# Optimization experiments

Hardware: AMD Instinct MI355X
Metric: run time of the kernel (lower is better)

The kernel has to match this reference:

```python
import jax, jax.numpy as jnp
import numpy as np

IN_DIM = 128
MEM = 128
BRANCH = 8
DEPTH = 6
N = (BRANCH ** (DEPTH + 1) - 1) // (BRANCH - 1)  # 299593 nodes, BFS order


def setup_inputs() -> dict:
    key = jax.random.key(0)
    ks = jax.random.split(key, 9)
    s_in = 1.0 / np.sqrt(IN_DIM)
    s_m = 1.0 / np.sqrt(MEM)
    f32 = jnp.float32
    return {
        "x": jax.random.normal(ks[0], (N, IN_DIM), f32),
        "W_ioux": jax.random.normal(ks[1], (3 * MEM, IN_DIM), f32) * s_in,
        "b_ioux": jax.random.normal(ks[2], (3 * MEM,), f32) * s_in,
        "W_iouh": jax.random.normal(ks[3], (3 * MEM, MEM), f32) * s_m,
        "b_iouh": jax.random.normal(ks[4], (3 * MEM,), f32) * s_m,
        "W_fx": jax.random.normal(ks[5], (MEM, IN_DIM), f32) * s_in,
        "b_fx": jax.random.normal(ks[6], (MEM,), f32) * s_in,
        "W_fh": jax.random.normal(ks[7], (MEM, MEM), f32) * s_m,
        "b_fh": jax.random.normal(ks[8], (MEM,), f32) * s_m,
        "branch": BRANCH,
        "depth": DEPTH,
    }


def reference(x, W_ioux, b_ioux, W_iouh, b_iouh, W_fx, b_fx, W_fh, b_fh, branch, depth):
    """Child-Sum TreeLSTM over a complete `branch`-ary tree of `depth` levels.

    Nodes are stored in BFS order: level l occupies [off(l), off(l+1)) and the
    children of local parent p at level l are contiguous at level l+1, so the
    recursion becomes a bottom-up sweep with one batched step per level.
    Matches torch node_forward exactly (leaf nodes see a single zero child row,
    i.e. h_sum = 0 -> iouh contributes only its bias, and fc_sum = 0).
    """
    mem = W_fh.shape[0]
    off = lambda l: (branch ** l - 1) // (branch - 1)
    c_prev = h_prev = None  # states of level l+1, [branch**(l+1), mem]
    for l in range(depth, -1, -1):
        n_l = branch ** l
        x_l = x[off(l): off(l) + n_l]  # [n_l, in_dim]
        if l == depth:  # leaves
            h_sum = jnp.zeros((n_l, mem), x.dtype)
            fc_sum = jnp.zeros((n_l, mem), x.dtype)
        else:
            c_ch = c_prev.reshape(n_l, branch, mem)
            h_ch = h_prev.reshape(n_l, branch, mem)
            h_sum = h_ch.sum(axis=1)  # child-sum of h
            # per-child forget gate: sigmoid(fh(h_child) + fx(x_parent))
            f = jax.nn.sigmoid(
                jnp.einsum('nbm,km->nbk', h_ch, W_fh) + b_fh
                + (x_l @ W_fx.T + b_fx)[:, None, :]
            )
            fc_sum = (f * c_ch).sum(axis=1)
        iou = x_l @ W_ioux.T + b_ioux + h_sum @ W_iouh.T + b_iouh
        i, o, u = jnp.split(iou, 3, axis=1)
        c_prev = jax.nn.sigmoid(i) * jnp.tanh(u) + fc_sum
        h_prev = jax.nn.sigmoid(o) * jnp.tanh(c_prev)
    return (c_prev, h_prev)  # root state, each [1, mem]
```

## Files before the change

### kernel.cpp

```cpp
#include <hip/hip_runtime.h>
#include <hip/hip_bf16.h>

#define TB 256
#define LOG2E  1.44269504088896f
#define LOG2E2 2.88539008177793f

typedef __attribute__((ext_vector_type(8))) short bf16x8;
typedef __attribute__((ext_vector_type(4))) float f32x4;

__device__ __forceinline__ short bfb(float f){
  unsigned u = __float_as_uint(f);
  u = u + 0x7fffu + ((u >> 16) & 1u);
  return (short)(u >> 16);
}
__device__ __forceinline__ bf16x8 cvt8(float4 a, float4 b){
  bf16x8 r;
  r[0]=bfb(a.x); r[1]=bfb(a.y); r[2]=bfb(a.z); r[3]=bfb(a.w);
  r[4]=bfb(b.x); r[5]=bfb(b.y); r[6]=bfb(b.z); r[7]=bfb(b.w);
  return r;
}
__device__ __forceinline__ float sig2(float arg){
  return __builtin_amdgcn_rcpf(1.f + __builtin_amdgcn_exp2f(arg));
}
__device__ __forceinline__ float tanh2(float arg){
  return 1.f - 2.f*__builtin_amdgcn_rcpf(1.f + __builtin_amdgcn_exp2f(arg));
}

#define GLD16(gp, lp) __builtin_amdgcn_global_load_lds( \
    (const __attribute__((address_space(1))) void*)(gp), \
    (__attribute__((address_space(3))) void*)(lp), 16, 0, 0)

__global__ __launch_bounds__(TB)
void k_prep(const float* __restrict__ Wioux, const float* __restrict__ Wiouh,
            const float* __restrict__ Wfx,   const float* __restrict__ Wfh,
            const float* __restrict__ bioux, const float* __restrict__ biouh,
            short* __restrict__ WxG, short* __restrict__ WhG,
            short* __restrict__ WfxP, short* __restrict__ WfhP,
            float* __restrict__ biasS){
  const int q = blockIdx.x*TB + threadIdx.x;
  const int t = q >> 8, rem = q & 255;
  const int kf = rem >> 6, lane = rem & 63;
  const int row = t*16 + (lane & 15);
  const int col = kf*32 + (lane >> 4)*8;
  const size_t src = (size_t)row*128 + col;
  if (q < 6144){
    const int g = t & 7, kind = t >> 3;
    const size_t dst = ((size_t)(g*3 + kind)*4 + kf)*512 + (size_t)lane*8;
    const float4* p  = (const float4*)(Wioux + src);
    *(bf16x8*)(WxG + dst) = cvt8(p[0], p[1]);
    const float4* p2 = (const float4*)(Wiouh + src);
    *(bf16x8*)(WhG + dst) = cvt8(p2[0], p2[1]);
  }
  if (q < 2048){
    const size_t dst = ((size_t)t*4 + kf)*512 + (size_t)lane*8;
    const float4* p  = (const float4*)(Wfx + src);
    *(bf16x8*)(WfxP + dst) = cvt8(p[0], p[1]);
    const float4* p2 = (const float4*)(Wfh + src);
    *(bf16x8*)(WfhP + dst) = cvt8(p2[0], p2[1]);
  }
  if (q < 384){
    const float s = (q < 256) ? -LOG2E : LOG2E2;
    biasS[q] = s*(bioux[q] + biouh[q]);
  }
}

__global__ __launch_bounds__(TB, 4)
void k_fx(const float* __restrict__ x, const short* __restrict__ WfxP,
          const float* __restrict__ bfx, const float* __restrict__ bfh,
          float* __restrict__ FXS, int nrows){
  const int tid = threadIdx.x, wave = tid >> 6, lane = tid & 63;
  const int l15 = lane & 15, lhi = lane >> 4;
  const int mrow = (blockIdx.x*4 + wave)*16;
  const int arow = min(mrow + l15, nrows - 1);
  bf16x8 ax[4];
  const float* rp = x + (size_t)arow*128;
  #pragma unroll
  for (int kf = 0; kf < 4; ++kf){
    const float4* p = (const float4*)(rp + kf*32 + lhi*8);
    ax[kf] = cvt8(p[0], p[1]);
  }
  #pragma unroll
  for (int t = 0; t < 8; ++t){
    f32x4 acc = {0.f,0.f,0.f,0.f};
    #pragma unroll
    for (int kf = 0; kf < 4; ++kf){
      bf16x8 b = *(const bf16x8*)(WfxP + ((size_t)(t*4 + kf)*64 + lane)*8);
      acc = __builtin_amdgcn_mfma_f32_16x16x32_bf16(ax[kf], b, acc, 0,0,0);
    }
    const int col = t*16 + l15;
    const float bc = bfx[col] + bfh[col];
    #pragma unroll
    for (int r = 0; r < 4; ++r){
      const int row = mrow + lhi*4 + r;
      if (row < nrows) FXS[(size_t)row*128 + col] = -LOG2E*(acc[r] + bc);
    }
  }
}

__global__ __launch_bounds__(TB, 4)
void k_leaf(const float* __restrict__ x, int xoff,
            const short* __restrict__ WxG, const short* __restrict__ WfhP,
            const float* __restrict__ biasS, const float* __restrict__ FXS,
            int poff, short* __restrict__ HSout, float* __restrict__ FCout)
{
  __shared__ __align__(16) short wbuf[2][6144];
  __shared__ __align__(16) short hbuf[4][2048];
  const int tid = threadIdx.x;
  const int wave = tid >> 6, lane = tid & 63;
  const int l15 = lane & 15, lhi = lane >> 4;
  const int mrow = (blockIdx.x*4 + wave)*16;

  bf16x8 ax[4];
  {
    const float* rp = x + (size_t)(xoff + mrow + l15)*128;
    #pragma unroll
    for (int kf = 0; kf < 4; ++kf){
      const float4* p = (const float4*)(rp + kf*32 + lhi*8);
      ax[kf] = cvt8(p[0], p[1]);
    }
  }

  #define STAGE_L(g, b) { \
    _Pragma("unroll") \
    for (int c = 0; c < 3; ++c){ \
      const int ch = c*4 + wave; \
      GLD16(WxG + (size_t)(g)*6144 + ch*512 + lane*8, &wbuf[b][ch*512]); \
    } }

  STAGE_L(0, 0);

  float cv[8][4];
  const int colb = l15*2;
  const int p = (mrow >> 3) + (lhi >> 1);
  const float* fxp = FXS + (size_t)(poff + p)*128 + l15;

  #pragma unroll
  for (int tt = 0; tt < 8; ++tt){
    __syncthreads();
    if (tt < 7) STAGE_L(tt+1, (tt+1)&1);
    const short* wb = wbuf[tt & 1];

    f32x4 ai = {0.f,0.f,0.f,0.f}, ao = ai, au = ai;
    #pragma unroll
    for (int kf = 0; kf < 4; ++kf){
      bf16x8 bi = *(const bf16x8*)(wb + 0*2048 + kf*512 + lane*8);
      bf16x8 bo = *(const bf16x8*)(wb + 1*2048 + kf*512 + lane*8);
      bf16x8 bu = *(const bf16x8*)(wb + 2*2048 + kf*512 + lane*8);
      ai = __builtin_amdgcn_mfma_f32_16x16x32_bf16(ax[kf], bi, ai, 0,0,0);
      ao = __builtin_amdgcn_mfma_f32_16x16x32_bf16(ax[kf], bo, ao, 0,0,0);
      au = __builtin_amdgcn_mfma_f32_16x16x32_bf16(ax[kf], bu, au, 0,0,0);
    }

    const int col = tt*16 + l15;
    const float bis = biasS[col], bos = biasS[128 + col], bus = biasS[256 + col];
    const int colx = colb + tt*32;
    float hs = 0.f;
    #pragma unroll
    for (int r = 0; r < 4; ++r){
      const int row = lhi*4 + r;
      const float iv = sig2 (__builtin_fmaf(ai[r], -LOG2E, bis));
      const float uv = tanh2(__builtin_fmaf(au[r],  LOG2E2, bus));
      const float ov = sig2 (__builtin_fmaf(ao[r], -LOG2E, bos));
      const float c  = iv*uv;
      const float h  = ov*tanh2(LOG2E2*c);
      cv[tt][r] = c;
      hs += h;
      const int byte = row*256 + (colx ^ (row << 4));
      *(short*)((char*)hbuf[wave] + byte) = bfb(h);
    }
    hs += __shfl_xor(hs, 16);
    if ((lhi & 1) == 0)
      HSout[(size_t)p*128 + col] = bfb(hs);
  }

  bf16x8 af[4];
  #pragma unroll
  for (int kf = 0; kf < 4; ++kf){
    const int byte = l15*256 + (((kf*32 + lhi*8)*2) ^ (l15 << 4));
    af[kf] = *(const bf16x8*)((const char*)hbuf[wave] + byte);
  }
  #pragma unroll
  for (int t2 = 0; t2 < 8; ++t2){
    f32x4 fa = {0.f,0.f,0.f,0.f};
    #pragma unroll
    for (int kf = 0; kf < 4; ++kf){
      bf16x8 b = *(const bf16x8*)(WfhP + ((size_t)(t2*4 + kf)*64 + lane)*8);
      fa = __builtin_amdgcn_mfma_f32_16x16x32_bf16(af[kf], b, fa, 0,0,0);
    }
    const float fxv = fxp[t2*16];
    float fs = 0.f;
    #pragma unroll
    for (int r = 0; r < 4; ++r){
      const float f = sig2(__builtin_fmaf(fa[r], -LOG2E, fxv));
      fs += f * cv[t2][r];
    }
    fs += __shfl_xor(fs, 16);
    if ((lhi & 1) == 0)
      FCout[(size_t)p*128 + t2*16 + l15] = fs;
  }
  #undef STAGE_L
}

__global__ __launch_bounds__(TB, 2)
void k_node(const float* __restrict__ x, int xoff,
            const short* __restrict__ HSin, const float* __restrict__ FCin,
            const short* __restrict__ WxG, const short* __restrict__ WhG,
            const short* __restrict__ WfhP,
            const float* __restrict__ biasS, const float* __restrict__ FXS,
            int poff, short* __restrict__ HSout, float* __restrict__ FCout,
            float* __restrict__ dout, int nnodes)
{
  __shared__ __align__(16) short wbuf[2][12288];
  __shared__ __align__(16) short hbuf[4][2048];
  const int tid = threadIdx.x;
  const int wave = tid >> 6, lane = tid & 63;
  const int l15 = lane & 15, lhi = lane >> 4;
  const int mrow = (blockIdx.x*4 + wave)*16;
  const int arow = min(mrow + l15, nnodes - 1);

  bf16x8 ax[4], ah[4];
  {
    const float* rp = x + (size_t)(xoff + arow)*128;
    #pragma unroll
    for (int kf = 0; kf < 4; ++kf){
      const float4* p = (const float4*)(rp + kf*32 + lhi*8);
      ax[kf] = cvt8(p[0], p[1]);
    }
    const short* hp = HSin + (size_t)arow*128;
    #pragma unroll
    for (int kf = 0; kf < 4; ++kf)
      ah[kf] = *(const bf16x8*)(hp + kf*32 + lhi*8);
  }

  #define STAGE_N(g, b) { \
    _Pragma("unroll") \
    for (int c = 0; c < 3; ++c){ \
      const int ch = c*4 + wave; \
      GLD16(WxG + (size_t)(g)*6144 + ch*512 + lane*8, &wbuf[b][ch*512]); \
      GLD16(WhG + (size_t)(g)*6144 + ch*512 + lane*8, &wbuf[b][6144 + ch*512]); \
    } }

  STAGE_N(0, 0);

  float cv[8][4];
  const int colb = l15*2;
  const int p = (min(mrow, nnodes - 1) >> 3) + (lhi >> 1);
  const float* fxp = FXS + (size_t)(poff + min(p, (nnodes - 1) >> 3))*128 + l15;

  #pragma unroll
  for (int tt = 0; tt < 8; ++tt){
    __syncthreads();
    if (tt < 7) STAGE_N(tt+1, (tt+1)&1);
    const short* wb = wbuf[tt & 1];

    f32x4 ai = {0.f,0.f,0.f,0.f}, ao = ai, au = ai;
    #pragma unroll
    for (int kf = 0; kf < 4; ++kf){
      bf16x8 bi = *(const bf16x8*)(wb + 0*2048 + kf*512 + lane*8);
      bf16x8 bo = *(const bf16x8*)(wb + 1*2048 + kf*512 + lane*8);
      bf16x8 bu = *(const bf16x8*)(wb + 2*2048 + kf*512 + lane*8);
      ai = __builtin_amdgcn_mfma_f32_16x16x32_bf16(ax[kf], bi, ai, 0,0,0);
      ao = __builtin_amdgcn_mfma_f32_16x16x32_bf16(ax[kf], bo, ao, 0,0,0);
      au = __builtin_amdgcn_mfma_f32_16x16x32_bf16(ax[kf], bu, au, 0,0,0);
    }
    #pragma unroll
    for (int kf = 0; kf < 4; ++kf){
      bf16x8 bi = *(const bf16x8*)(wb + 6144 + 0*2048 + kf*512 + lane*8);
      bf16x8 bo = *(const bf16x8*)(wb + 6144 + 1*2048 + kf*512 + lane*8);
      bf16x8 bu = *(const bf16x8*)(wb + 6144 + 2*2048 + kf*512 + lane*8);
      ai = __builtin_amdgcn_mfma_f32_16x16x32_bf16(ah[kf], bi, ai, 0,0,0);
      ao = __builtin_amdgcn_mfma_f32_16x16x32_bf16(ah[kf], bo, ao, 0,0,0);
      au = __builtin_amdgcn_mfma_f32_16x16x32_bf16(ah[kf], bu, au, 0,0,0);
    }

    const int col = tt*16 + l15;
    const float bis = biasS[col], bos = biasS[128 + col], bus = biasS[256 + col];
    const int colx = colb + tt*32;
    float hs = 0.f;
    #pragma unroll
    for (int r = 0; r < 4; ++r){
      const int row = lhi*4 + r;
      const int loc = min(mrow + row, nnodes - 1);
      const float fc = FCin[(size_t)loc*128 + col];
      const float iv = sig2 (__builtin_fmaf(ai[r], -LOG2E, bis));
      const float uv = tanh2(__builtin_fmaf(au[r],  LOG2E2, bus));
      const float ov = sig2 (__builtin_fmaf(ao[r], -LOG2E, bos));
      const float c  = __builtin_fmaf(iv, uv, fc);
      const float h  = ov*tanh2(LOG2E2*c);
      cv[tt][r] = c;
      hs += h;
      const int byte = row*256 + (colx ^ (row << 4));
      *(short*)((char*)hbuf[wave] + byte) = bfb(h);
      if (dout && (mrow + row) == 0){ dout[col] = c; dout[128 + col] = h; }
    }
    if (HSout){
      hs += __shfl_xor(hs, 16);
      if ((lhi & 1) == 0){
        const int pv = (lhi == 0) ? (mrow < nnodes) : (mrow + 8 < nnodes);
        if (pv) HSout[(size_t)p*128 + col] = bfb(hs);
      }
    }
  }

  if (!HSout) return;

  bf16x8 af[4];
  #pragma unroll
  for (int kf = 0; kf < 4; ++kf){
    const int byte = l15*256 + (((kf*32 + lhi*8)*2) ^ (l15 << 4));
    af[kf] = *(const bf16x8*)((const char*)hbuf[wave] + byte);
  }
  #pragma unroll
  for (int t2 = 0; t2 < 8; ++t2){
    f32x4 fa = {0.f,0.f,0.f,0.f};
    #pragma unroll
    for (int kf = 0; kf < 4; ++kf){
      bf16x8 b = *(const bf16x8*)(WfhP + ((size_t)(t2*4 + kf)*64 + lane)*8);
      fa = __builtin_amdgcn_mfma_f32_16x16x32_bf16(af[kf], b, fa, 0,0,0);
    }
    const float fxv = fxp[t2*16];
    float fs = 0.f;
    #pragma unroll
    for (int r = 0; r < 4; ++r){
      const float f = sig2(__builtin_fmaf(fa[r], -LOG2E, fxv));
      fs += f * cv[t2][r];
    }
    fs += __shfl_xor(fs, 16);
    if ((lhi & 1) == 0){
      const int pv = (lhi == 0) ? (mrow < nnodes) : (mrow + 8 < nnodes);
      if (pv) FCout[(size_t)p*128 + t2*16 + l15] = fs;
    }
  }
  #undef STAGE_N
}

extern "C" void kernel_launch(void* const* d_in, const int* in_sizes, int n_in,
                              void* d_out, int out_size, void* d_ws, size_t ws_size,
                              hipStream_t stream)
{
  const float* x     = (const float*)d_in[0];
  const float* Wioux = (const float*)d_in[1];
  const float* bioux = (const float*)d_in[2];
  const float* Wiouh = (const float*)d_in[3];
  const float* biouh = (const float*)d_in[4];
  const float* Wfx   = (const float*)d_in[5];
  const float* bfx   = (const float*)d_in[6];
  const float* Wfh   = (const float*)d_in[7];
  const float* bfh   = (const float*)d_in[8];
  float* dout = (float*)d_out;

  static const int n_l[7]   = {1, 8, 64, 512, 4096, 32768, 262144};
  static const int off_l[7] = {0, 1, 9, 73, 585, 4681, 37449};

  char* base = (char*)d_ws;
  size_t off = 0;
  auto take = [&](size_t bytes)->char*{
    char* r = base + off;
    off = (off + bytes + 255) & ~(size_t)255;
    return r;
  };
  float* FXS  = (float*)take((size_t)37449*128*4);
  float* FC0  = (float*)take((size_t)32768*128*4);
  float* FC1  = (float*)take((size_t)32768*128*4);
  short* HS0  = (short*)take((size_t)32768*128*2);
  short* HS1  = (short*)take((size_t)32768*128*2);
  short* WxG  = (short*)take((size_t)24*2048*2);
  short* WhG  = (short*)take((size_t)24*2048*2);
  short* WfxP = (short*)take((size_t)8*2048*2);
  short* WfhP = (short*)take((size_t)8*2048*2);
  float* biasS= (float*)take((size_t)384*4);
  if (off > ws_size) return;

  short* HS[2] = {HS0, HS1};
  float* FC[2] = {FC0, FC1};

  k_prep<<<24, TB, 0, stream>>>(Wioux, Wiouh, Wfx, Wfh, bioux, biouh,
                                WxG, WhG, WfxP, WfhP, biasS);
  k_fx<<<(37449 + 63)/64, TB, 0, stream>>>(x, WfxP, bfx, bfh, FXS, 37449);

  k_leaf<<<262144/64, TB, 0, stream>>>(x, off_l[6], WxG, WfhP, biasS, FXS,
                                       off_l[5], HS1, FC1);

  for (int l = 5; l >= 0; --l){
    const int n = n_l[l];
    const int grid = (n + 63)/64;
    k_node<<<grid, TB, 0, stream>>>(
      x, off_l[l], HS[l & 1], FC[l & 1],
      WxG, WhG, WfhP, biasS, FXS,
      (l > 0) ? off_l[l-1] : 0,
      (l > 0) ? HS[(l & 1) ^ 1] : nullptr,
      (l > 0) ? FC[(l & 1) ^ 1] : nullptr,
      (l == 0) ? dout : nullptr, n);
  }
}
```

Measured before the change: 193.5 us.

## Double leaf rows per wave and fuse top three tree levels into one kernel

The leaf kernel now processes 32 rows per wave with two A fragments, so each staged LDS weight tile feeds twice as many MFMAs. The c and h values are packed to bf16 in registers, and occupancy drops to 3 blocks per CU. The last three levels (64, 8 and 1 nodes) run in a single one-block kernel with __syncthreads between levels, which removes two launches. The tail reads weights straight from global memory and stores c in bf16, which lowers the precision of the forget-gate product.

```diff
diff --git a/kernel.cpp b/kernel.cpp
--- a/kernel.cpp
+++ b/kernel.cpp
@@ -97,7 +97,7 @@
   }
 }
 
-__global__ __launch_bounds__(TB, 4)
+__global__ __launch_bounds__(TB, 3)
 void k_leaf(const float* __restrict__ x, int xoff,
             const short* __restrict__ WxG, const short* __restrict__ WfhP,
             const float* __restrict__ biasS, const float* __restrict__ FXS,
@@ -108,15 +108,18 @@
   const int tid = threadIdx.x;
   const int wave = tid >> 6, lane = tid & 63;
   const int l15 = lane & 15, lhi = lane >> 4;
-  const int mrow = (blockIdx.x*4 + wave)*16;
-
-  bf16x8 ax[4];
+  const int mrow = (blockIdx.x*4 + wave)*32;
+
+  bf16x8 ax0[4], ax1[4];
   {
-    const float* rp = x + (size_t)(xoff + mrow + l15)*128;
-    #pragma unroll
-    for (int kf = 0; kf < 4; ++kf){
-      const float4* p = (const float4*)(rp + kf*32 + lhi*8);
-      ax[kf] = cvt8(p[0], p[1]);
+    const float* rp0 = x + (size_t)(xoff + mrow + l15)*128;
+    const float* rp1 = rp0 + 16*128;
+    #pragma unroll
+    for (int kf = 0; kf < 4; ++kf){
+      const float4* p0 = (const float4*)(rp0 + kf*32 + lhi*8);
+      ax0[kf] = cvt8(p0[0], p0[1]);
+      const float4* p1 = (const float4*)(rp1 + kf*32 + lhi*8);
+      ax1[kf] = cvt8(p1[0], p1[1]);
     }
   }
 
@@ -129,10 +132,9 @@
 
   STAGE_L(0, 0);
 
-  float cv[8][4];
-  const int colb = l15*2;
-  const int p = (mrow >> 3) + (lhi >> 1);
-  const float* fxp = FXS + (size_t)(poff + p)*128 + l15;
+  unsigned cpk0[8][2], cpk1[8][2], hpk0[8][2], hpk1[8][2];
+  const int p0 = (mrow >> 3) + (lhi >> 1);
+  const int p1 = ((mrow + 16) >> 3) + (lhi >> 1);
 
   #pragma unroll
   for (int tt = 0; tt < 8; ++tt){
@@ -140,64 +142,98 @@
     if (tt < 7) STAGE_L(tt+1, (tt+1)&1);
     const short* wb = wbuf[tt & 1];
 
-    f32x4 ai = {0.f,0.f,0.f,0.f}, ao = ai, au = ai;
+    f32x4 ai0 = {0.f,0.f,0.f,0.f}, ao0 = ai0, au0 = ai0;
+    f32x4 ai1 = ai0, ao1 = ai0, au1 = ai0;
     #pragma unroll
     for (int kf = 0; kf < 4; ++kf){
       bf16x8 bi = *(const bf16x8*)(wb + 0*2048 + kf*512 + lane*8);
       bf16x8 bo = *(const bf16x8*)(wb + 1*2048 + kf*512 + lane*8);
       bf16x8 bu = *(const bf16x8*)(wb + 2*2048 + kf*512 + lane*8);
-      ai = __builtin_amdgcn_mfma_f32_16x16x32_bf16(ax[kf], bi, ai, 0,0,0);
-      ao = __builtin_amdgcn_mfma_f32_16x16x32_bf16(ax[kf], bo, ao, 0,0,0);
-      au = __builtin_amdgcn_mfma_f32_16x16x32_bf16(ax[kf], bu, au, 0,0,0);
+      ai0 = __builtin_amdgcn_mfma_f32_16x16x32_bf16(ax0[kf], bi, ai0, 0,0,0);
+      ai1 = __builtin_amdgcn_mfma_f32_16x16x32_bf16(ax1[kf], bi, ai1, 0,0,0);
+      ao0 = __builtin_amdgcn_mfma_f32_16x16x32_bf16(ax0[kf], bo, ao0, 0,0,0);
+      ao1 = __builtin_amdgcn_mfma_f32_16x16x32_bf16(ax1[kf], bo, ao1, 0,0,0);
+      au0 = __builtin_amdgcn_mfma_f32_16x16x32_bf16(ax0[kf], bu, au0, 0,0,0);
+      au1 = __builtin_amdgcn_mfma_f32_16x16x32_bf16(ax1[kf], bu, au1, 0,0,0);
     }
 
     const int col = tt*16 + l15;
     const float bis = biasS[col], bos = biasS[128 + col], bus = biasS[256 + col];
-    const int colx = colb + tt*32;
-    float hs = 0.f;
-    #pragma unroll
-    for (int r = 0; r < 4; ++r){
-      const int row = lhi*4 + r;
-      const float iv = sig2 (__builtin_fmaf(ai[r], -LOG2E, bis));
-      const float uv = tanh2(__builtin_fmaf(au[r],  LOG2E2, bus));
-      const float ov = sig2 (__builtin_fmaf(ao[r], -LOG2E, bos));
-      const float c  = iv*uv;
-      const float h  = ov*tanh2(LOG2E2*c);
-      cv[tt][r] = c;
-      hs += h;
-      const int byte = row*256 + (colx ^ (row << 4));
-      *(short*)((char*)hbuf[wave] + byte) = bfb(h);
-    }
-    hs += __shfl_xor(hs, 16);
-    if ((lhi & 1) == 0)
-      HSout[(size_t)p*128 + col] = bfb(hs);
-  }
-
-  bf16x8 af[4];
-  #pragma unroll
-  for (int kf = 0; kf < 4; ++kf){
-    const int byte = l15*256 + (((kf*32 + lhi*8)*2) ^ (l15 << 4));
-    af[kf] = *(const bf16x8*)((const char*)hbuf[wave] + byte);
-  }
-  #pragma unroll
-  for (int t2 = 0; t2 < 8; ++t2){
-    f32x4 fa = {0.f,0.f,0.f,0.f};
-    #pragma unroll
-    for (int kf = 0; kf < 4; ++kf){
-      bf16x8 b = *(const bf16x8*)(WfhP + ((size_t)(t2*4 + kf)*64 + lane)*8);
-      fa = __builtin_amdgcn_mfma_f32_16x16x32_bf16(af[kf], b, fa, 0,0,0);
-    }
-    const float fxv = fxp[t2*16];
-    float fs = 0.f;
-    #pragma unroll
-    for (int r = 0; r < 4; ++r){
-      const float f = sig2(__builtin_fmaf(fa[r], -LOG2E, fxv));
-      fs += f * cv[t2][r];
-    }
-    fs += __shfl_xor(fs, 16);
-    if ((lhi & 1) == 0)
-      FCout[(size_t)p*128 + t2*16 + l15] = fs;
-  }
+
+    #define GATES_L(AI, AO, AU, CPK, HPK, P) { \
+      float hs = 0.f; \
+      _Pragma("unroll") \
+      for (int q = 0; q < 2; ++q){ \
+        unsigned cp = 0, hp = 0; \
+        _Pragma("unroll") \
+        for (int s = 0; s < 2; ++s){ \
+          const int r = q*2 + s; \
+          const float iv = sig2 (__builtin_fmaf(AI[r], -LOG2E, bis)); \
+          const float uv = tanh2(__builtin_fmaf(AU[r],  LOG2E2, bus)); \
+          const float ov = sig2 (__builtin_fmaf(AO[r], -LOG2E, bos)); \
+          const float c  = iv*uv; \
+          const float hv = ov*tanh2(LOG2E2*c); \
+          hs += hv; \
+          cp |= (unsigned)(unsigned short)bfb(c)  << (16*s); \
+          hp |= (unsigned)(unsigned short)bfb(hv) << (16*s); \
+        } \
+        CPK[tt][q] = cp; HPK[tt][q] = hp; \
+      } \
+      hs += __shfl_xor(hs, 16); \
+      if ((lhi & 1) == 0) HSout[(size_t)(P)*128 + col] = bfb(hs); \
+    }
+
+    GATES_L(ai0, ao0, au0, cpk0, hpk0, p0);
+    GATES_L(ai1, ao1, au1, cpk1, hpk1, p1);
+    #undef GATES_L
+  }
+
+  #define FH_L(CPK, HPK, P) { \
+    _Pragma("unroll") \
+    for (int t2 = 0; t2 < 8; ++t2){ \
+      _Pragma("unroll") \
+      for (int q = 0; q < 2; ++q){ \
+        const unsigned v = HPK[t2][q]; \
+        const int r0 = lhi*4 + q*2, r1 = r0 + 1; \
+        const int cx = t2*32 + l15*2; \
+        *(short*)((char*)hbuf[wave] + r0*256 + (cx ^ (r0 << 4))) = (short)v; \
+        *(short*)((char*)hbuf[wave] + r1*256 + (cx ^ (r1 << 4))) = (short)(v >> 16); \
+      } \
+    } \
+    bf16x8 af[4]; \
+    _Pragma("unroll") \
+    for (int kf = 0; kf < 4; ++kf){ \
+      const int byte = l15*256 + (((kf*32 + lhi*8)*2) ^ (l15 << 4)); \
+      af[kf] = *(const bf16x8*)((const char*)hbuf[wave] + byte); \
+    } \
+    const float* fxp = FXS + (size_t)(poff + (P))*128 + l15; \
+    _Pragma("unroll") \
+    for (int t2 = 0; t2 < 8; ++t2){ \
+      f32x4 fa = {0.f,0.f,0.f,0.f}; \
+      _Pragma("unroll") \
+      for (int kf = 0; kf < 4; ++kf){ \
+        bf16x8 b = *(const bf16x8*)(WfhP + ((size_t)(t2*4 + kf)*64 + lane)*8); \
+        fa = __builtin_amdgcn_mfma_f32_16x16x32_bf16(af[kf], b, fa, 0,0,0); \
+      } \
+      const float fxv = fxp[t2*16]; \
+      float fs = 0.f; \
+      _Pragma("unroll") \
+      for (int q = 0; q < 2; ++q){ \
+        const unsigned cp = CPK[t2][q]; \
+        const float c0 = __uint_as_float(cp << 16); \
+        const float c1 = __uint_as_float(cp & 0xffff0000u); \
+        const float f0 = sig2(__builtin_fmaf(fa[q*2],     -LOG2E, fxv)); \
+        const float f1 = sig2(__builtin_fmaf(fa[q*2 + 1], -LOG2E, fxv)); \
+        fs += f0*c0 + f1*c1; \
+      } \
+      fs += __shfl_xor(fs, 16); \
+      if ((lhi & 1) == 0) FCout[(size_t)(P)*128 + t2*16 + l15] = fs; \
+    } \
+  }
+
+  FH_L(cpk0, hpk0, p0);
+  FH_L(cpk1, hpk1, p1);
+  #undef FH_L
   #undef STAGE_L
 }
 
@@ -208,7 +244,7 @@
             const short* __restrict__ WfhP,
             const float* __restrict__ biasS, const float* __restrict__ FXS,
             int poff, short* __restrict__ HSout, float* __restrict__ FCout,
-            float* __restrict__ dout, int nnodes)
+            int nnodes)
 {
   __shared__ __align__(16) short wbuf[2][12288];
   __shared__ __align__(16) short hbuf[4][2048];
@@ -291,6 +327,112 @@
       hs += h;
       const int byte = row*256 + (colx ^ (row << 4));
       *(short*)((char*)hbuf[wave] + byte) = bfb(h);
+    }
+    hs += __shfl_xor(hs, 16);
+    if ((lhi & 1) == 0){
+      const int pv = (lhi == 0) ? (mrow < nnodes) : (mrow + 8 < nnodes);
+      if (pv) HSout[(size_t)p*128 + col] = bfb(hs);
+    }
+  }
+
+  bf16x8 af[4];
+  #pragma unroll
+  for (int kf = 0; kf < 4; ++kf){
+    const int byte = l15*256 + (((kf*32 + lhi*8)*2) ^ (l15 << 4));
+    af[kf] = *(const bf16x8*)((const char*)hbuf[wave] + byte);
+  }
+  #pragma unroll
+  for (int t2 = 0; t2 < 8; ++t2){
+    f32x4 fa = {0.f,0.f,0.f,0.f};
+    #pragma unroll
+    for (int kf = 0; kf < 4; ++kf){
+      bf16x8 b = *(const bf16x8*)(WfhP + ((size_t)(t2*4 + kf)*64 + lane)*8);
+      fa = __builtin_amdgcn_mfma_f32_16x16x32_bf16(af[kf], b, fa, 0,0,0);
+    }
+    const float fxv = fxp[t2*16];
+    float fs = 0.f;
+    #pragma unroll
+    for (int r = 0; r < 4; ++r){
+      const float f = sig2(__builtin_fmaf(fa[r], -LOG2E, fxv));
+      fs += f * cv[t2][r];
+    }
+    fs += __shfl_xor(fs, 16);
+    if ((lhi & 1) == 0){
+      const int pv = (lhi == 0) ? (mrow < nnodes) : (mrow + 8 < nnodes);
+      if (pv) FCout[(size_t)p*128 + t2*16 + l15] = fs;
+    }
+  }
+  #undef STAGE_N
+}
+
+__device__ __forceinline__ void tail_level(
+    const float* __restrict__ x, int xoff,
+    const short* __restrict__ HSin, const float* __restrict__ FCin,
+    const short* __restrict__ WxG, const short* __restrict__ WhG,
+    const short* __restrict__ WfhP,
+    const float* __restrict__ biasS, const float* __restrict__ FXS, int poff,
+    short* __restrict__ HSout, float* __restrict__ FCout,
+    float* __restrict__ dout, int nnodes, short* __restrict__ hb)
+{
+  const int tid = threadIdx.x;
+  const int lane = tid & 63;
+  const int l15 = lane & 15, lhi = lane >> 4;
+  const int mrow = (tid >> 6)*16;
+  const int arow = min(mrow + l15, nnodes - 1);
+
+  bf16x8 ax[4], ah[4];
+  {
+    const float* rp = x + (size_t)(xoff + arow)*128;
+    #pragma unroll
+    for (int kf = 0; kf < 4; ++kf){
+      const float4* p = (const float4*)(rp + kf*32 + lhi*8);
+      ax[kf] = cvt8(p[0], p[1]);
+    }
+    const short* hp = HSin + (size_t)arow*128;
+    #pragma unroll
+    for (int kf = 0; kf < 4; ++kf)
+      ah[kf] = *(const bf16x8*)(hp + kf*32 + lhi*8);
+  }
+
+  float cv[8][4];
+  const int p = (min(mrow, nnodes - 1) >> 3) + (lhi >> 1);
+  const float* fxp = FXS + (size_t)(poff + min(p, (nnodes - 1) >> 3))*128 + l15;
+
+  #pragma unroll
+  for (int tt = 0; tt < 8; ++tt){
+    f32x4 ai = {0.f,0.f,0.f,0.f}, ao = ai, au = ai;
+    #pragma unroll
+    for (int kf = 0; kf < 4; ++kf){
+      bf16x8 bxi = *(const bf16x8*)(WxG + ((size_t)(tt*3 + 0)*4 + kf)*512 + lane*8);
+      bf16x8 bxo = *(const bf16x8*)(WxG + ((size_t)(tt*3 + 1)*4 + kf)*512 + lane*8);
+      bf16x8 bxu = *(const bf16x8*)(WxG + ((size_t)(tt*3 + 2)*4 + kf)*512 + lane*8);
+      ai = __builtin_amdgcn_mfma_f32_16x16x32_bf16(ax[kf], bxi, ai, 0,0,0);
+      ao = __builtin_amdgcn_mfma_f32_16x16x32_bf16(ax[kf], bxo, ao, 0,0,0);
+      au = __builtin_amdgcn_mfma_f32_16x16x32_bf16(ax[kf], bxu, au, 0,0,0);
+      bf16x8 bhi = *(const bf16x8*)(WhG + ((size_t)(tt*3 + 0)*4 + kf)*512 + lane*8);
+      bf16x8 bho = *(const bf16x8*)(WhG + ((size_t)(tt*3 + 1)*4 + kf)*512 + lane*8);
+      bf16x8 bhu = *(const bf16x8*)(WhG + ((size_t)(tt*3 + 2)*4 + kf)*512 + lane*8);
+      ai = __builtin_amdgcn_mfma_f32_16x16x32_bf16(ah[kf], bhi, ai, 0,0,0);
+      ao = __builtin_amdgcn_mfma_f32_16x16x32_bf16(ah[kf], bho, ao, 0,0,0);
+      au = __builtin_amdgcn_mfma_f32_16x16x32_bf16(ah[kf], bhu, au, 0,0,0);
+    }
+    const int col = tt*16 + l15;
+    const float bis = biasS[col], bos = biasS[128 + col], bus = biasS[256 + col];
+    float hs = 0.f;
+    #pragma unroll
+    for (int r = 0; r < 4; ++r){
+      const int row = lhi*4 + r;
+      const int loc = min(mrow + row, nnodes - 1);
+      const float fc = FCin[(size_t)loc*128 + col];
+      const float iv = sig2 (__builtin_fmaf(ai[r], -LOG2E, bis));
+      const float uv = tanh2(__builtin_fmaf(au[r],  LOG2E2, bus));
+      const float ov = sig2 (__builtin_fmaf(ao[r], -LOG2E, bos));
+      const float c  = __builtin_fmaf(iv, uv, fc);
+      const float h  = ov*tanh2(LOG2E2*c);
+      cv[tt][r] = c;
+      hs += h;
+      const int byte = row*256 + ((l15*2 + tt*32) ^ (row << 4));
+      *(short*)((char*)hb + byte) = bfb(h);
       if (dout && (mrow + row) == 0){ dout[col] = c; dout[128 + col] = h; }
     }
     if (HSout){
@@ -301,14 +443,13 @@
       }
     }
   }
-
   if (!HSout) return;
 
   bf16x8 af[4];
   #pragma unroll
   for (int kf = 0; kf < 4; ++kf){
     const int byte = l15*256 + (((kf*32 + lhi*8)*2) ^ (l15 << 4));
-    af[kf] = *(const bf16x8*)((const char*)hbuf[wave] + byte);
+    af[kf] = *(const bf16x8*)((const char*)hb + byte);
   }
   #pragma unroll
   for (int t2 = 0; t2 < 8; ++t2){
@@ -331,7 +472,24 @@
       if (pv) FCout[(size_t)p*128 + t2*16 + l15] = fs;
     }
   }
-  #undef STAGE_N
+}
+
+__global__ __launch_bounds__(TB, 1)
+void k_tail(const float* __restrict__ x,
+            const short* __restrict__ WxG, const short* __restrict__ WhG,
+            const short* __restrict__ WfhP,
+            const float* __restrict__ biasS, const float* __restrict__ FXS,
+            short* __restrict__ HS0, short* __restrict__ HS1,
+            float* __restrict__ FC0, float* __restrict__ FC1,
+            float* __restrict__ dout)
+{
+  __shared__ __align__(16) short hbuf[4][2048];
+  short* hb = hbuf[threadIdx.x >> 6];
+  tail_level(x, 9, HS0, FC0, WxG, WhG, WfhP, biasS, FXS, 1, HS1, FC1, nullptr, 64, hb);
+  __syncthreads();
+  tail_level(x, 1, HS1, FC1, WxG, WhG, WfhP, biasS, FXS, 0, HS0, FC0, nullptr, 8, hb);
+  __syncthreads();
+  tail_level(x, 0, HS0, FC0, WxG, WhG, WfhP, biasS, FXS, 0, nullptr, nullptr, dout, 1, hb);
 }
 
 extern "C" void kernel_launch(void* const* d_in, const int* in_sizes, int n_in,
@@ -378,18 +536,16 @@
                                 WxG, WhG, WfxP, WfhP, biasS);
   k_fx<<<(37449 + 63)/64, TB, 0, stream>>>(x, WfxP, bfx, bfh, FXS, 37449);
 
-  k_leaf<<<262144/64, TB, 0, stream>>>(x, off_l[6], WxG, WfhP, biasS, FXS,
-                                       off_l[5], HS1, FC1);
-
-  for (int l = 5; l >= 0; --l){
+  k_leaf<<<262144/128, TB, 0, stream>>>(x, off_l[6], WxG, WfhP, biasS, FXS,
+                                        off_l[5], HS1, FC1);
+
+  for (int l = 5; l >= 3; --l){
     const int n = n_l[l];
-    const int grid = (n + 63)/64;
-    k_node<<<grid, TB, 0, stream>>>(
+    k_node<<<(n + 63)/64, TB, 0, stream>>>(
       x, off_l[l], HS[l & 1], FC[l & 1],
       WxG, WhG, WfhP, biasS, FXS,
-      (l > 0) ? off_l[l-1] : 0,
-      (l > 0) ? HS[(l & 1) ^ 1] : nullptr,
-      (l > 0) ? FC[(l & 1) ^ 1] : nullptr,
-      (l == 0) ? dout : nullptr, n);
-  }
-}
+      off_l[l-1], HS[(l & 1) ^ 1], FC[(l & 1) ^ 1], n);
+  }
+  k_tail<<<1, TB, 0, stream>>>(x, WxG, WhG, WfhP, biasS, FXS,
+                               HS0, HS1, FC0, FC1, dout);
+}
```

Result: slower. 284.1 us (+46.8%).

## Reuse weight LDS for h staging, pack states to bf16, fuse top levels into one kernel

Applied to the files above, without the earlier changes.

The leaf and node kernels no longer keep a separate LDS buffer for h. They pack h (and in the leaf kernel also c) into bf16 register pairs and write h into the now-free weight staging buffer after a barrier. This lowers LDS and register use so launch bounds can rise to 5 and 3 blocks per SM. The three smallest levels (64, 8 and 1 nodes) run in a single one-block tail kernel that reads weights directly from global memory, which removes two launches. The leaf cell state is now kept in bf16, which costs some precision in the forget-gate sum.

```diff
diff --git a/kernel.cpp b/kernel.cpp
--- a/kernel.cpp
+++ b/kernel.cpp
@@ -97,14 +97,13 @@
   }
 }
 
-__global__ __launch_bounds__(TB, 4)
+__global__ __launch_bounds__(TB, 5)
 void k_leaf(const float* __restrict__ x, int xoff,
             const short* __restrict__ WxG, const short* __restrict__ WfhP,
             const float* __restrict__ biasS, const float* __restrict__ FXS,
             int poff, short* __restrict__ HSout, float* __restrict__ FCout)
 {
   __shared__ __align__(16) short wbuf[2][6144];
-  __shared__ __align__(16) short hbuf[4][2048];
   const int tid = threadIdx.x;
   const int wave = tid >> 6, lane = tid & 63;
   const int l15 = lane & 15, lhi = lane >> 4;
@@ -129,8 +128,7 @@
 
   STAGE_L(0, 0);
 
-  float cv[8][4];
-  const int colb = l15*2;
+  unsigned cpk[8][2], hpk[8][2];
   const int p = (mrow >> 3) + (lhi >> 1);
   const float* fxp = FXS + (size_t)(poff + p)*128 + l15;
 
@@ -153,31 +151,46 @@
 
     const int col = tt*16 + l15;
     const float bis = biasS[col], bos = biasS[128 + col], bus = biasS[256 + col];
-    const int colx = colb + tt*32;
     float hs = 0.f;
     #pragma unroll
-    for (int r = 0; r < 4; ++r){
-      const int row = lhi*4 + r;
-      const float iv = sig2 (__builtin_fmaf(ai[r], -LOG2E, bis));
-      const float uv = tanh2(__builtin_fmaf(au[r],  LOG2E2, bus));
-      const float ov = sig2 (__builtin_fmaf(ao[r], -LOG2E, bos));
-      const float c  = iv*uv;
-      const float h  = ov*tanh2(LOG2E2*c);
-      cv[tt][r] = c;
-      hs += h;
-      const int byte = row*256 + (colx ^ (row << 4));
-      *(short*)((char*)hbuf[wave] + byte) = bfb(h);
+    for (int q = 0; q < 2; ++q){
+      unsigned cp = 0, hp = 0;
+      #pragma unroll
+      for (int s = 0; s < 2; ++s){
+        const int r = q*2 + s;
+        const float iv = sig2 (__builtin_fmaf(ai[r], -LOG2E, bis));
+        const float uv = tanh2(__builtin_fmaf(au[r],  LOG2E2, bus));
+        const float ov = sig2 (__builtin_fmaf(ao[r], -LOG2E, bos));
+        const float c  = iv*uv;
+        const float hv = ov*tanh2(LOG2E2*c);
+        hs += hv;
+        cp |= (unsigned)(unsigned short)bfb(c)  << (16*s);
+        hp |= (unsigned)(unsigned short)bfb(hv) << (16*s);
+      }
+      cpk[tt][q] = cp; hpk[tt][q] = hp;
     }
     hs += __shfl_xor(hs, 16);
-    if ((lhi & 1) == 0)
-      HSout[(size_t)p*128 + col] = bfb(hs);
-  }
-
+    if ((lhi & 1) == 0) HSout[(size_t)p*128 + col] = bfb(hs);
+  }
+
+  __syncthreads();
+  short* hb = ((short*)wbuf) + wave*2048;
+  #pragma unroll
+  for (int t2 = 0; t2 < 8; ++t2){
+    #pragma unroll
+    for (int q = 0; q < 2; ++q){
+      const unsigned v = hpk[t2][q];
+      const int r0 = lhi*4 + q*2, r1 = r0 + 1;
+      const int cx = t2*32 + l15*2;
+      *(short*)((char*)hb + r0*256 + (cx ^ (r0 << 4))) = (short)v;
+      *(short*)((char*)hb + r1*256 + (cx ^ (r1 << 4))) = (short)(v >> 16);
+    }
+  }
   bf16x8 af[4];
   #pragma unroll
   for (int kf = 0; kf < 4; ++kf){
     const int byte = l15*256 + (((kf*32 + lhi*8)*2) ^ (l15 << 4));
-    af[kf] = *(const bf16x8*)((const char*)hbuf[wave] + byte);
+    af[kf] = *(const bf16x8*)((const char*)hb + byte);
   }
   #pragma unroll
   for (int t2 = 0; t2 < 8; ++t2){
@@ -190,28 +203,30 @@
     const float fxv = fxp[t2*16];
     float fs = 0.f;
     #pragma unroll
-    for (int r = 0; r < 4; ++r){
-      const float f = sig2(__builtin_fmaf(fa[r], -LOG2E, fxv));
-      fs += f * cv[t2][r];
+    for (int q = 0; q < 2; ++q){
+      const unsigned cp = cpk[t2][q];
+      const float c0 = __uint_as_float(cp << 16);
+      const float c1 = __uint_as_float(cp & 0xffff0000u);
+      const float f0 = sig2(__builtin_fmaf(fa[q*2],     -LOG2E, fxv));
+      const float f1 = sig2(__builtin_fmaf(fa[q*2 + 1], -LOG2E, fxv));
+      fs += f0*c0 + f1*c1;
     }
     fs += __shfl_xor(fs, 16);
-    if ((lhi & 1) == 0)
-      FCout[(size_t)p*128 + t2*16 + l15] = fs;
+    if ((lhi & 1) == 0) FCout[(size_t)p*128 + t2*16 + l15] = fs;
   }
   #undef STAGE_L
 }
 
-__global__ __launch_bounds__(TB, 2)
+__global__ __launch_bounds__(TB, 3)
 void k_node(const float* __restrict__ x, int xoff,
             const short* __restrict__ HSin, const float* __restrict__ FCin,
             const short* __restrict__ WxG, const short* __restrict__ WhG,
             const short* __restrict__ WfhP,
             const float* __restrict__ biasS, const float* __restrict__ FXS,
             int poff, short* __restrict__ HSout, float* __restrict__ FCout,
-            float* __restrict__ dout, int nnodes)
+            int nnodes)
 {
   __shared__ __align__(16) short wbuf[2][12288];
-  __shared__ __align__(16) short hbuf[4][2048];
   const int tid = threadIdx.x;
   const int wave = tid >> 6, lane = tid & 63;
   const int l15 = lane & 15, lhi = lane >> 4;
@@ -243,9 +258,9 @@
   STAGE_N(0, 0);
 
   float cv[8][4];
-  const int colb = l15*2;
-  const int p = (min(mrow, nnodes - 1) >> 3) + (lhi >> 1);
-  const float* fxp = FXS + (size_t)(poff + min(p, (nnodes - 1) >> 3))*128 + l15;
+  unsigned hpk[8][2];
+  const int p = (mrow >> 3) + (lhi >> 1);
+  const float* fxp = FXS + (size_t)(poff + p)*128 + l15;
 
   #pragma unroll
   for (int tt = 0; tt < 8; ++tt){
@@ -275,7 +290,122 @@
 
     const int col = tt*16 + l15;
     const float bis = biasS[col], bos = biasS[128 + col], bus = biasS[256 + col];
-    const int colx = colb + tt*32;
+    float hs = 0.f;
+    #pragma unroll
+    for (int q = 0; q < 2; ++q){
+      unsigned hp = 0;
+      #pragma unroll
+      for (int s = 0; s < 2; ++s){
+        const int r = q*2 + s;
+        const float fc = FCin[(size_t)(mrow + lhi*4 + r)*128 + col];
+        const float iv = sig2 (__builtin_fmaf(ai[r], -LOG2E, bis));
+        const float uv = tanh2(__builtin_fmaf(au[r],  LOG2E2, bus));
+        const float ov = sig2 (__builtin_fmaf(ao[r], -LOG2E, bos));
+        const float c  = __builtin_fmaf(iv, uv, fc);
+        const float hv = ov*tanh2(LOG2E2*c);
+        cv[tt][r] = c;
+        hs += hv;
+        hp |= (unsigned)(unsigned short)bfb(hv) << (16*s);
+      }
+      hpk[tt][q] = hp;
+    }
+    hs += __shfl_xor(hs, 16);
+    if ((lhi & 1) == 0) HSout[(size_t)p*128 + col] = bfb(hs);
+  }
+
+  __syncthreads();
+  short* hb = ((short*)wbuf) + wave*2048;
+  #pragma unroll
+  for (int t2 = 0; t2 < 8; ++t2){
+    #pragma unroll
+    for (int q = 0; q < 2; ++q){
+      const unsigned v = hpk[t2][q];
+      const int r0 = lhi*4 + q*2, r1 = r0 + 1;
+      const int cx = t2*32 + l15*2;
+      *(short*)((char*)hb + r0*256 + (cx ^ (r0 << 4))) = (short)v;
+      *(short*)((char*)hb + r1*256 + (cx ^ (r1 << 4))) = (short)(v >> 16);
+    }
+  }
+  bf16x8 af[4];
+  #pragma unroll
+  for (int kf = 0; kf < 4; ++kf){
+    const int byte = l15*256 + (((kf*32 + lhi*8)*2) ^ (l15 << 4));
+    af[kf] = *(const bf16x8*)((const char*)hb + byte);
+  }
+  #pragma unroll
+  for (int t2 = 0; t2 < 8; ++t2){
+    f32x4 fa = {0.f,0.f,0.f,0.f};
+    #pragma unroll
+    for (int kf = 0; kf < 4; ++kf){
+      bf16x8 b = *(const bf16x8*)(WfhP + ((size_t)(t2*4 + kf)*64 + lane)*8);
+      fa = __builtin_amdgcn_mfma_f32_16x16x32_bf16(af[kf], b, fa, 0,0,0);
+    }
+    const float fxv = fxp[t2*16];
+    float fs = 0.f;
+    #pragma unroll
+    for (int r = 0; r < 4; ++r){
+      const float f = sig2(__builtin_fmaf(fa[r], -LOG2E, fxv));
+      fs += f * cv[t2][r];
+    }
+    fs += __shfl_xor(fs, 16);
+    if ((lhi & 1) == 0) FCout[(size_t)p*128 + t2*16 + l15] = fs;
+  }
+  #undef STAGE_N
+}
+
+__device__ __forceinline__ void tail_level(
+    const float* __restrict__ x, int xoff,
+    const short* __restrict__ HSin, const float* __restrict__ FCin,
+    const short* __restrict__ WxG, const short* __restrict__ WhG,
+    const short* __restrict__ WfhP,
+    const float* __restrict__ biasS, const float* __restrict__ FXS, int poff,
+    short* __restrict__ HSout, float* __restrict__ FCout,
+    float* __restrict__ dout, int nnodes, short* __restrict__ hb)
+{
+  const int tid = threadIdx.x;
+  const int lane = tid & 63;
+  const int l15 = lane & 15, lhi = lane >> 4;
+  const int mrow = (tid >> 6)*16;
+  const int arow = min(mrow + l15, nnodes - 1);
+
+  bf16x8 ax[4], ah[4];
+  {
+    const float* rp = x + (size_t)(xoff + arow)*128;
+    #pragma unroll
+    for (int kf = 0; kf < 4; ++kf){
+      const float4* p = (const float4*)(rp + kf*32 + lhi*8);
+      ax[kf] = cvt8(p[0], p[1]);
+    }
+    const short* hp = HSin + (size_t)arow*128;
+    #pragma unroll
+    for (int kf = 0; kf < 4; ++kf)
+      ah[kf] = *(const bf16x8*)(hp + kf*32 + lhi*8);
+  }
+
+  float cv[8][4];
+  const int p = (min(mrow, nnodes - 1) >> 3) + (lhi >> 1);
+  const float* fxp = FXS + (size_t)(poff + min(p, (nnodes - 1) >> 3))*128 + l15;
+
+  #pragma unroll
+  for (int tt = 0; tt < 8; ++tt){
+    f32x4 ai = {0.f,0.f,0.f,0.f}, ao = ai, au = ai;
+    #pragma unroll
+    for (int kf = 0; kf < 4; ++kf){
+      bf16x8 bxi = *(const bf16x8*)(WxG + ((size_t)(tt*3 + 0)*4 + kf)*512 + lane*8);
+      bf16x8 bxo = *(const bf16x8*)(WxG + ((size_t)(tt*3 + 1)*4 + kf)*512 + lane*8);
+      bf16x8 bxu = *(const bf16x8*)(WxG + ((size_t)(tt*3 + 2)*4 + kf)*512 + lane*8);
+      ai = __builtin_amdgcn_mfma_f32_16x16x32_bf16(ax[kf], bxi, ai, 0,0,0);
+      ao = __builtin_amdgcn_mfma_f32_16x16x32_bf16(ax[kf], bxo, ao, 0,0,0);
+      au = __builtin_amdgcn_mfma_f32_16x16x32_bf16(ax[kf], bxu, au, 0,0,0);
+      bf16x8 bhi = *(const bf16x8*)(WhG + ((size_t)(tt*3 + 0)*4 + kf)*512 + lane*8);
+      bf16x8 bho = *(const bf16x8*)(WhG + ((size_t)(tt*3 + 1)*4 + kf)*512 + lane*8);
+      bf16x8 bhu = *(const bf16x8*)(WhG + ((size_t)(tt*3 + 2)*4 + kf)*512 + lane*8);
+      ai = __builtin_amdgcn_mfma_f32_16x16x32_bf16(ah[kf], bhi, ai, 0,0,0);
+      ao = __builtin_amdgcn_mfma_f32_16x16x32_bf16(ah[kf], bho, ao, 0,0,0);
+      au = __builtin_amdgcn_mfma_f32_16x16x32_bf16(ah[kf], bhu, au, 0,0,0);
+    }
+    const int col = tt*16 + l15;
+    const float bis = biasS[col], bos = biasS[128 + col], bus = biasS[256 + col];
     float hs = 0.f;
     #pragma unroll
     for (int r = 0; r < 4; ++r){
@@ -289,8 +419,8 @@
       const float h  = ov*tanh2(LOG2E2*c);
       cv[tt][r] = c;
       hs += h;
-      const int byte = row*256 + (colx ^ (row << 4));
-      *(short*)((char*)hbuf[wave] + byte) = bfb(h);
+      const int byte = row*256 + ((l15*2 + tt*32) ^ (row << 4));
+      *(short*)((char*)hb + byte) = bfb(h);
       if (dout && (mrow + row) == 0){ dout[col] = c; dout[128 + col] = h; }
     }
     if (HSout){
@@ -301,14 +431,13 @@
       }
     }
   }
-
   if (!HSout) return;
 
   bf16x8 af[4];
   #pragma unroll
   for (int kf = 0; kf < 4; ++kf){
     const int byte = l15*256 + (((kf*32 + lhi*8)*2) ^ (l15 << 4));
-    af[kf] = *(const bf16x8*)((const char*)hbuf[wave] + byte);
+    af[kf] = *(const bf16x8*)((const char*)hb + byte);
   }
   #pragma unroll
   for (int t2 = 0; t2 < 8; ++t2){
@@ -331,7 +460,24 @@
       if (pv) FCout[(size_t)p*128 + t2*16 + l15] = fs;
     }
   }
-  #undef STAGE_N
+}
+
+__global__ __launch_bounds__(TB, 1)
+void k_tail(const float* __restrict__ x,
+            const short* __restrict__ WxG, const short* __restrict__ WhG,
+            const short* __restrict__ WfhP,
+            const float* __restrict__ biasS, const float* __restrict__ FXS,
+            short* __restrict__ HS0, short* __restrict__ HS1,
+            float* __restrict__ FC0, float* __restrict__ FC1,
+            float* __restrict__ dout)
+{
+  __shared__ __align__(16) short hbuf[4][2048];
+  short* hb = hbuf[threadIdx.x >> 6];
+  tail_level(x, 9, HS0, FC0, WxG, WhG, WfhP, biasS, FXS, 1, HS1, FC1, nullptr, 64, hb);
+  __syncthreads();
+  tail_level(x, 1, HS1, FC1, WxG, WhG, WfhP, biasS, FXS, 0, HS0, FC0, nullptr, 8, hb);
+  __syncthreads();
+  tail_level(x, 0, HS0, FC0, WxG, WhG, WfhP, biasS, FXS, 0, nullptr, nullptr, dout, 1, hb);
 }
 
 extern "C" void kernel_launch(void* const* d_in, const int* in_sizes, int n_in,
@@ -381,15 +527,13 @@
   k_leaf<<<262144/64, TB, 0, stream>>>(x, off_l[6], WxG, WfhP, biasS, FXS,
                                        off_l[5], HS1, FC1);
 
-  for (int l = 5; l >= 0; --l){
+  for (int l = 5; l >= 3; --l){
     const int n = n_l[l];
-    const int grid = (n + 63)/64;
-    k_node<<<grid, TB, 0, stream>>>(
+    k_node<<<(n + 63)/64, TB, 0, stream>>>(
       x, off_l[l], HS[l & 1], FC[l & 1],
       WxG, WhG, WfhP, biasS, FXS,
-      (l > 0) ? off_l[l-1] : 0,
-      (l > 0) ? HS[(l & 1) ^ 1] : nullptr,
-      (l > 0) ? FC[(l & 1) ^ 1] : nullptr,
-      (l == 0) ? dout : nullptr, n);
-  }
-}
+      off_l[l-1], HS[(l & 1) ^ 1], FC[(l & 1) ^ 1], n);
+  }
+  k_tail<<<1, TB, 0, stream>>>(x, WxG, WhG, WfhP, biasS, FXS,
+                               HS0, HS1, FC0, FC1, dout);
+}
```

Measured after the change: 216.7 us. +12.0%, slower.
